# Kernel optimization log

Measured on AMD Instinct MI355X. Metric: run time of the kernel, lower is better.

The kernel has to match this reference:

```python
import math
import jax, jax.numpy as jnp
import numpy as np

ROUNDS = 4
BUCKET_LEN = 64
NEG_BIG = -1e9
NEG_SELF = -1e5
EPS = 1e-12


def look_back(x):
    # x: [B, n_buckets, bucket_len, ...]; prepend previous bucket (circular) along bucket_len axis
    return jnp.concatenate([jnp.roll(x, 1, axis=1), x], axis=2)


def gather_dim1(x, idx):
    # torch expand_gather: broadcast x and idx to common shape, gather along axis 1
    shape = np.broadcast_shapes(x.shape, idx.shape)
    return jnp.take_along_axis(jnp.broadcast_to(x, shape), jnp.broadcast_to(idx, shape), axis=1)


def setup_inputs() -> dict:
    key = jax.random.key(0)
    k1, k2, k3 = jax.random.split(key, 3)
    B, L, d_k = 16, 4096, 64
    n_buckets = L // BUCKET_LEN
    query = jax.random.normal(k1, (B, L, d_k), dtype=jnp.float32)
    value = jax.random.normal(k2, (B, L, d_k), dtype=jnp.float32)
    rand_matrix = jax.random.normal(k3, (B, d_k, ROUNDS, n_buckets // 2), dtype=jnp.float32)
    return {"query": query, "value": value, "rand_matrix": rand_matrix, "seed": 0}


def lsh_hashes(query, rand_matrix):
    # LocalitySensitiveHash.forward
    B, L, d_k = query.shape
    qn = query / jnp.maximum(jnp.linalg.norm(query, axis=-1, keepdims=True), EPS)
    rm = rand_matrix / jnp.linalg.norm(rand_matrix, axis=1, keepdims=True)
    mm = jnp.einsum('bld,bdrn->blrn', qn, rm)  # [B, L, rounds, n_buckets//2]
    h = jnp.argmax(jnp.concatenate([mm, -mm], axis=-1), axis=-1).astype(jnp.int32)  # [B, L, rounds]
    return h * L + jnp.arange(L, dtype=jnp.int32)[None, :, None]  # unique per position


def _lsh_attention(query, value, rand_matrix):
    B, L, d_k = query.shape
    R, bl = ROUNDS, BUCKET_LEN
    nb = L // bl

    h = lsh_hashes(query, rand_matrix)
    sorted_hashes = jnp.sort(h, axis=1)
    hash_indice = jnp.argsort(h, axis=1)               # [B, L, R]
    original_indice = jnp.argsort(hash_indice, axis=1)  # reverse_sort

    # reorder queries by hash, bucketize: [B, nb, bl, d_k, R]
    rq = gather_dim1(query[:, :, :, None], hash_indice[:, :, None, :]).reshape(B, nb, bl, d_k, R)
    lb_key = look_back(rq)
    lb_key = lb_key / jnp.maximum(jnp.linalg.norm(lb_key, axis=-2, keepdims=True), EPS)
    scores = jnp.einsum('bnidr,bnjdr->bnijr', rq, lb_key) / math.sqrt(d_k)  # [B, nb, bl, 2bl, R]

    # mask: different buckets, causal, self
    sh = sorted_hashes.reshape(B, nb, bl, R) // L  # bucket id
    scores = jnp.where(sh[..., None, :] != look_back(sh)[..., None, :, :], NEG_BIG, scores)
    qi = hash_indice.reshape(B, nb, bl, R).astype(jnp.int32)
    ki = look_back(qi)  # [B, nb, 2bl, R]
    scores = jnp.where(qi[..., None, :] < ki[..., None, :, :], NEG_BIG, scores)
    scores = jnp.where(qi[..., None, :] == ki[..., None, :, :], NEG_SELF, scores)

    # duplicate-key counting across rounds (get_dup_keys)
    ki_full = jnp.broadcast_to(ki[:, :, None, :, :], (B, nb, bl, 2 * bl, R)).reshape(B, L, 2 * bl, R)
    ki_full = gather_dim1(ki_full, original_indice[:, :, None, :])
    flat = ki_full.reshape(B, L, 2 * bl * R)
    s_idx = jnp.argsort(flat, axis=-1)
    s = jnp.take_along_axis(flat, s_idx, axis=-1)
    counts = jnp.ones_like(s)
    for i in range(1, R):
        eq = (s[..., i:] == s[..., :-i]).astype(s.dtype)
        counts = counts + jnp.pad(eq, ((0, 0), (0, 0), (i, 0))) + jnp.pad(eq, ((0, 0), (0, 0), (0, i)))
    inv = jnp.argsort(s_idx, axis=-1)
    count_key = jnp.take_along_axis(counts, inv, axis=-1).reshape(B, L, 2 * bl, R)
    count_key = gather_dim1(count_key, hash_indice[:, :, None, :])

    # duplicate-adjusted softmax
    scores = scores.reshape(B, L, 2 * bl, R)
    lse = jax.nn.logsumexp(scores, axis=2)  # [B, L, R]
    softmax_qk = jnp.exp(scores - jnp.log(count_key.astype(scores.dtype)) - lse[:, :, None, :])

    rv = gather_dim1(value[:, :, :, None], hash_indice[:, :, None, :]).reshape(B, nb, bl, d_k, R)
    sm = softmax_qk.reshape(B, nb, bl, 2 * bl, R)
    attn = jnp.einsum('bnijr,bnjdr->bnidr', sm, look_back(rv)).reshape(B, L, d_k, R)
    attn = gather_dim1(attn, original_indice[:, :, None, :])
    lse = jnp.take_along_axis(lse, original_indice, axis=1)
    round_weights = jax.nn.softmax(lse, axis=1)  # dim=1 (length) exactly as in the source
    return jnp.einsum('bldr,blr->bld', attn, round_weights)


def reference(query, value, rand_matrix, seed):
    # seed is unused by the original forward body; dropout skipped (eval mode)
    return _lsh_attention(query, value, rand_matrix)
```

## Files before the change

### kernel.cpp

```cpp
#include <hip/hip_runtime.h>
#include <math.h>

#define B_  16
#define L_  4096
#define D_  64
#define R_  4
#define NB_ 64
#define BL_ 64
#define FIXCAP 8192

typedef _Float16 f16x8 __attribute__((ext_vector_type(8)));
typedef _Float16 f16x2 __attribute__((ext_vector_type(2)));
typedef float    f32x4 __attribute__((ext_vector_type(4)));


__global__ __launch_bounds__(64) void k_rmnorm(const float* __restrict__ rm,
                                               double* __restrict__ rmn,
                                               _Float16* __restrict__ rhi_g,
                                               _Float16* __restrict__ rlo_g,
                                               int* __restrict__ fix_cnt) {
    if (blockIdx.x == 0 && threadIdx.x == 0) *fix_cnt = 0;
    int blk = blockIdx.x;
    int b = blk >> 7, r = (blk >> 5) & 3, n = blk & 31;
    int d = threadIdx.x;
    double v = (double)rm[(((size_t)b * 64 + d) * 4 + r) * 32 + n];
    double sq = v * v;
    #pragma unroll
    for (int off = 32; off > 0; off >>= 1) sq += __shfl_down(sq, off);
    double tot = __shfl(sq, 0);
    double nv = v / sqrt(tot);
    rmn[(((size_t)b * 4 + r) * 32 + n) * 64 + d] = nv;
    float f = (float)nv;
    _Float16 hi = (_Float16)f;
    size_t gi = ((size_t)b * 128 + r * 32 + n) * 64 + d;
    rhi_g[gi] = hi;
    rlo_g[gi] = (_Float16)(f - (float)hi);
}

__global__ __launch_bounds__(256, 4) void k_hash(const float* __restrict__ q,
                                                 const float* __restrict__ value,
                                                 const _Float16* __restrict__ rhi_g,
                                                 const _Float16* __restrict__ rlo_g,
                                                 int* __restrict__ h_ws,
                                                 int* __restrict__ fix_cnt,
                                                 int* __restrict__ fix_list,
                                                 _Float16* __restrict__ qhf,
                                                 _Float16* __restrict__ khf,
                                                 _Float16* __restrict__ vhf) {
    __shared__ __align__(16) char smem[36864];
    _Float16* Rhi = (_Float16*)smem;
    _Float16* Rlo = (_Float16*)(smem + 18432);
    float*    Sc  = (float*)smem;

    int blk = blockIdx.x;
    int b = blk >> 6, chunk = blk & 63;
    int tid = threadIdx.x;
    int w = tid >> 6, lane = tid & 63, quad = lane >> 4, l15 = lane & 15;

    {
        int row = chunk * 64 + (tid >> 2), sub = tid & 3;
        const float4* vp = (const float4*)(value + ((size_t)(b * L_ + row)) * 64 + sub * 16);
        f16x8 h0, h1;
        #pragma unroll
        for (int c = 0; c < 2; c++) {
            float4 t0 = vp[2 * c], t1 = vp[2 * c + 1];
            f16x8& hd = c ? h1 : h0;
            hd[0]=(_Float16)t0.x; hd[1]=(_Float16)t0.y; hd[2]=(_Float16)t0.z; hd[3]=(_Float16)t0.w;
            hd[4]=(_Float16)t1.x; hd[5]=(_Float16)t1.y; hd[6]=(_Float16)t1.z; hd[7]=(_Float16)t1.w;
        }
        _Float16* dst = vhf + ((size_t)(b * L_ + row)) * 64 + sub * 16;
        *(f16x8*)dst = h0;
        *(f16x8*)(dst + 8) = h1;
    }

    {
        int row = tid >> 1, dh = (tid & 1) * 32;
        const _Float16* sh = rhi_g + ((size_t)b * 128 + row) * 64 + dh;
        const _Float16* sl = rlo_g + ((size_t)b * 128 + row) * 64 + dh;
        #pragma unroll
        for (int g = 0; g < 4; g++) {
            *(f16x8*)&Rhi[row * 72 + dh + g * 8] = *(const f16x8*)(sh + g * 8);
            *(f16x8*)&Rlo[row * 72 + dh + g * 8] = *(const f16x8*)(sl + g * 8);
        }
    }

    int qrow = chunk * 64 + w * 16 + l15;
    const float* qp = q + ((size_t)(b * L_ + qrow)) * 64;
    float qv[16];
    #pragma unroll
    for (int kt = 0; kt < 2; kt++) {
        float4 t0 = *(const float4*)(qp + kt * 32 + quad * 8);
        float4 t1 = *(const float4*)(qp + kt * 32 + quad * 8 + 4);
        qv[8*kt+0]=t0.x; qv[8*kt+1]=t0.y; qv[8*kt+2]=t0.z; qv[8*kt+3]=t0.w;
        qv[8*kt+4]=t1.x; qv[8*kt+5]=t1.y; qv[8*kt+6]=t1.z; qv[8*kt+7]=t1.w;
    }
    f16x8 Ahi[2], Alo[2];
    #pragma unroll
    for (int kt = 0; kt < 2; kt++) {
        #pragma unroll
        for (int j = 0; j < 8; j++) {
            _Float16 hi = (_Float16)qv[8*kt+j];
            Ahi[kt][j] = hi;
            Alo[kt][j] = (_Float16)(qv[8*kt+j] - (float)hi);
        }
    }
    {
        float ss = 0.f;
        #pragma unroll
        for (int j = 0; j < 16; j++) ss += qv[j] * qv[j];
        ss += __shfl_xor(ss, 16);
        ss += __shfl_xor(ss, 32);
        float nr = sqrtf(ss); if (nr < 1e-12f) nr = 1e-12f;
        float kscale = 0.125f / nr;
        _Float16* qd = qhf + ((size_t)(b * L_ + qrow)) * 64;
        _Float16* kd = khf + ((size_t)(b * L_ + qrow)) * 64;
        #pragma unroll
        for (int kt = 0; kt < 2; kt++) {
            *(f16x8*)(qd + kt * 32 + quad * 8) = Ahi[kt];
            f16x8 hv;
            #pragma unroll
            for (int j = 0; j < 8; j++) hv[j] = (_Float16)(qv[8*kt+j] * kscale);
            *(f16x8*)(kd + kt * 32 + quad * 8) = hv;
        }
    }
    __syncthreads();

    f32x4 acc[8];
    #pragma unroll
    for (int jt = 0; jt < 8; jt++) acc[jt] = (f32x4){0.f, 0.f, 0.f, 0.f};
    #pragma unroll
    for (int jt = 0; jt < 8; jt++) {
        #pragma unroll
        for (int kt = 0; kt < 2; kt++) {
            f16x8 bh = *(const f16x8*)&Rhi[(jt * 16 + l15) * 72 + kt * 32 + quad * 8];
            f16x8 bl = *(const f16x8*)&Rlo[(jt * 16 + l15) * 72 + kt * 32 + quad * 8];
            acc[jt] = __builtin_amdgcn_mfma_f32_16x16x32_f16(Ahi[kt], bh, acc[jt], 0, 0, 0);
            acc[jt] = __builtin_amdgcn_mfma_f32_16x16x32_f16(Ahi[kt], bl, acc[jt], 0, 0, 0);
            acc[jt] = __builtin_amdgcn_mfma_f32_16x16x32_f16(Alo[kt], bh, acc[jt], 0, 0, 0);
        }
    }
    __syncthreads();

    #pragma unroll
    for (int jt = 0; jt < 8; jt++) {
        #pragma unroll
        for (int reg = 0; reg < 4; reg++)
            Sc[(w * 16 + quad * 4 + reg) * 133 + jt * 16 + l15] = acc[jt][reg];
    }
    __syncthreads();

    {
        int row = tid & 63, r = tid >> 6;
        const float* sp = &Sc[row * 133 + r * 32];
        float bp = -1e30f, bn = -1e30f; int ip = 0, in2 = 0;
        float v1 = -1e30f, v2 = -1e30f;
        #pragma unroll
        for (int n = 0; n < 32; n++) {
            float v = sp[n], nv = -v;
            if (v > bp)  { bp = v;  ip = n; }
            if (nv > bn) { bn = nv; in2 = n; }
            if (v > v1)       { v2 = v1; v1 = v; }
            else if (v > v2)  { v2 = v; }
            if (nv > v1)      { v2 = v1; v1 = nv; }
            else if (nv > v2) { v2 = nv; }
        }
        int i1 = (bp >= bn) ? ip : (32 + in2);
        int l = chunk * 64 + row;
        h_ws[((size_t)(b * 4 + r)) * L_ + l] = i1;
        if (v1 - v2 < 4e-5f) {
            int slot = atomicAdd(fix_cnt, 1);
            if (slot < FIXCAP) fix_list[slot] = (b << 14) | (r << 12) | l;
        }
    }
}

__global__ __launch_bounds__(64) void k_fix(const float* __restrict__ q,
                                            const double* __restrict__ rmn,
                                            const int* __restrict__ fix_cnt,
                                            const int* __restrict__ fix_list,
                                            int* __restrict__ h_ws) {
    int cnt = *fix_cnt; if (cnt > FIXCAP) cnt = FIXCAP;
    int lane = threadIdx.x;
    for (int i = blockIdx.x; i < cnt; i += gridDim.x) {
        int e = fix_list[i];
        int b = e >> 14, r = (e >> 12) & 3, l = e & 4095;
        int n = lane & 31;
        const double* rp = rmn + ((size_t)(b * 4 + r)) * 2048 + n * 64;
        const float* qr = q + ((size_t)(b * L_ + l)) * 64;
        double a0 = 0.0, a1 = 0.0, a2 = 0.0, a3 = 0.0;
        #pragma unroll
        for (int d = 0; d < 64; d += 4) {
            a0 += (double)qr[d]   * rp[d];
            a1 += (double)qr[d+1] * rp[d+1];
            a2 += (double)qr[d+2] * rp[d+2];
            a3 += (double)qr[d+3] * rp[d+3];
        }
        double acc = ((a0 + a1) + (a2 + a3));
        double v = (lane < 32) ? acc : -acc;
        int idx = lane;
        #pragma unroll
        for (int off = 1; off < 64; off <<= 1) {
            double ov = __shfl_xor(v, off);
            int   oidx = __shfl_xor(idx, off);
            if (ov > v || (ov == v && oidx < idx)) { v = ov; idx = oidx; }
        }
        if (lane == 0) h_ws[((size_t)(b * 4 + r)) * L_ + l] = idx;
    }
}

__global__ __launch_bounds__(64) void k_sort(const int* __restrict__ h_ws,
                                             int* __restrict__ hi_ws,
                                             int* __restrict__ oi_ws) {
    __shared__ int hs[64 * 65];
    __shared__ int cnt[64 * 65];
    int br = blockIdx.x;
    const int* hp = h_ws + (size_t)br * L_;
    int t = threadIdx.x;
    for (int w = 0; w < 64; w++) hs[w * 65 + t] = hp[w * 64 + t];
    for (int u = 0; u < 64; u++) cnt[t * 65 + u] = 0;
    __syncthreads();
    for (int k = 0; k < 64; k++) cnt[t * 65 + hs[t * 65 + k]]++;
    __syncthreads();
    int cs = 0;
    for (int c = 0; c < 64; c++) cs += cnt[c * 65 + t];
    int v = cs;
    #pragma unroll
    for (int off = 1; off < 64; off <<= 1) {
        int u = __shfl_up(v, off);
        if (t >= off) v += u;
    }
    int running = v - cs;
    for (int c = 0; c < 64; c++) {
        int tmp = cnt[c * 65 + t];
        cnt[c * 65 + t] = running;
        running += tmp;
    }
    __syncthreads();
    int* hi = hi_ws + (size_t)br * L_;
    int* oi = oi_ws + (size_t)br * L_;
    for (int k = 0; k < 64; k++) {
        int idx = t * 64 + k;
        int b2 = hs[t * 65 + k];
        int pos = cnt[t * 65 + b2]++;
        hi[pos] = idx;
        oi[idx] = pos;
    }
}

__global__ __launch_bounds__(256) void k_meta(const int* __restrict__ h_ws,
                                              const int* __restrict__ hi_ws,
                                              const int* __restrict__ oi_ws,
                                              int4* __restrict__ meta_ws) {
    int gid = blockIdx.x * 256 + threadIdx.x;
    int br = gid >> 12, spos = gid & 4095;
    int b = br >> 2;
    int p = hi_ws[(size_t)br * L_ + spos];
    int hh = h_ws[(size_t)br * L_ + p];
    int pack = 0, packm1 = 0;
    #pragma unroll
    for (int r2 = 0; r2 < 4; r2++) {
        int bk = oi_ws[((size_t)(b * 4 + r2)) * L_ + p] >> 6;
        pack   |= bk << (8 * r2);
        packm1 |= ((bk + 63) & 63) << (8 * r2);
    }
    meta_ws[(size_t)br * L_ + spos] = make_int4(hh, p, pack, packm1);
}

__global__ __launch_bounds__(256, 4) void k_attn(const _Float16* __restrict__ qhf,
                                                 const _Float16* __restrict__ khf,
                                                 const _Float16* __restrict__ vhf,
                                                 const int4* __restrict__ meta_ws,
                                                 float* __restrict__ lse_ws,
                                                 _Float16* __restrict__ attn_ws) {
    __shared__ _Float16 Ksh[128 * 72];
    __shared__ _Float16 Vt[64 * 136];
    __shared__ int4 kmeta[128];

    int xcd = blockIdx.x & 7, slot = blockIdx.x >> 3;
    int b = xcd * 2 + (slot >> 8);
    int rem = slot & 255, n = rem >> 2, r = rem & 3;
    int tid = threadIdx.x;
    int w = tid >> 6, lane = tid & 63, quad = lane >> 4, l15 = lane & 15;
    int hibase = (b * 4 + r) * L_;

    if (tid < 128) {
        int j = tid;
        int nprev = (n + 63) & 63;
        int spos = (j < 64) ? (nprev * 64 + j) : (n * 64 + (j - 64));
        kmeta[j] = meta_ws[hibase + spos];
    }
    __syncthreads();

    {
        int j = tid >> 1, dh = (tid & 1) * 32;
        const _Float16* src = khf + ((size_t)(b * L_ + kmeta[j].y)) * 64 + dh;
        #pragma unroll
        for (int g = 0; g < 4; g++)
            *(f16x8*)&Ksh[j * 72 + dh + g * 8] = *(const f16x8*)(src + g * 8);
    }
    {
        int m = tid >> 2, sub = tid & 3;
        const _Float16* v0 = vhf + ((size_t)(b * L_ + kmeta[2 * m].y)) * 64 + sub * 16;
        const _Float16* v1 = vhf + ((size_t)(b * L_ + kmeta[2 * m + 1].y)) * 64 + sub * 16;
        f16x8 a00 = *(const f16x8*)v0, a01 = *(const f16x8*)(v0 + 8);
        f16x8 a10 = *(const f16x8*)v1, a11 = *(const f16x8*)(v1 + 8);
        #pragma unroll
        for (int d = 0; d < 8; d++) {
            f16x2 hv = { a00[d], a10[d] };
            *(f16x2*)&Vt[(sub * 16 + d) * 136 + 2 * m] = hv;
            f16x2 hw = { a01[d], a11[d] };
            *(f16x2*)&Vt[(sub * 16 + 8 + d) * 136 + 2 * m] = hw;
        }
    }

    int4 qmw = kmeta[64 + w * 16 + l15];
    const _Float16* qp = qhf + ((size_t)(b * L_ + qmw.y)) * 64;
    f16x8 afr[2];
    afr[0] = *(const f16x8*)(qp + quad * 8);
    afr[1] = *(const f16x8*)(qp + 32 + quad * 8);
    __syncthreads();

    f32x4 acc[8];
    #pragma unroll
    for (int jt = 0; jt < 8; jt++) acc[jt] = (f32x4){0.f, 0.f, 0.f, 0.f};
    #pragma unroll
    for (int jt = 0; jt < 8; jt++) {
        #pragma unroll
        for (int kt = 0; kt < 2; kt++) {
            f16x8 bfr = *(const f16x8*)&Ksh[(jt * 16 + l15) * 72 + kt * 32 + quad * 8];
            acc[jt] = __builtin_amdgcn_mfma_f32_16x16x32_f16(afr[kt], bfr, acc[jt], 0, 0, 0);
        }
    }

    int4 qm4[4], km4[8];
    #pragma unroll
    for (int reg = 0; reg < 4; reg++) qm4[reg] = kmeta[64 + w * 16 + quad * 4 + reg];
    #pragma unroll
    for (int jt = 0; jt < 8; jt++) km4[jt] = kmeta[jt * 16 + l15];
    __syncthreads();

    _Float16* Ph = Ksh;
    float lse_r[4];
    #pragma unroll
    for (int reg = 0; reg < 4; reg++) {
        float s[8];
        #pragma unroll
        for (int jt = 0; jt < 8; jt++) {
            float v = acc[jt][reg];
            if (km4[jt].x != qm4[reg].x) v = -1e9f;
            if (qm4[reg].y < km4[jt].y)  v = -1e9f;
            if (qm4[reg].y == km4[jt].y) v = -1e5f;
            s[jt] = v;
        }
        float m = s[0];
        #pragma unroll
        for (int jt = 1; jt < 8; jt++) m = fmaxf(m, s[jt]);
        #pragma unroll
        for (int off = 1; off < 16; off <<= 1) m = fmaxf(m, __shfl_xor(m, off));
        float te[8], sum = 0.f;
        #pragma unroll
        for (int jt = 0; jt < 8; jt++) { te[jt] = __expf(s[jt] - m); sum += te[jt]; }
        #pragma unroll
        for (int off = 1; off < 16; off <<= 1) sum += __shfl_xor(sum, off);
        float inv = __builtin_amdgcn_rcpf(sum);
        lse_r[reg] = m + __logf(sum);
        int i = w * 16 + quad * 4 + reg;
        #pragma unroll
        for (int jt = 0; jt < 8; jt++) {
            int z1 = km4[jt].z ^ qm4[reg].z;
            int z2 = km4[jt].z ^ qm4[reg].w;
            int nz = __popc((z1 + 0x7f7f7f7f) & 0x80808080)
                   + __popc((z2 + 0x7f7f7f7f) & 0x80808080);
            float p = te[jt] * inv * __builtin_amdgcn_rcpf((float)(8 - nz));
            Ph[i * 136 + jt * 16 + l15] = (_Float16)p;
        }
    }
    if (l15 == 0) {
        #pragma unroll
        for (int reg = 0; reg < 4; reg++)
            lse_ws[hibase + qm4[reg].y] = lse_r[reg];
    }
    __syncthreads();

    f32x4 oacc[4];
    #pragma unroll
    for (int nt = 0; nt < 4; nt++) oacc[nt] = (f32x4){0.f, 0.f, 0.f, 0.f};
    #pragma unroll
    for (int kt = 0; kt < 4; kt++) {
        f16x8 pa = *(const f16x8*)&Ph[(w * 16 + l15) * 136 + kt * 32 + quad * 8];
        #pragma unroll
        for (int nt = 0; nt < 4; nt++) {
            f16x8 vb = *(const f16x8*)&Vt[(nt * 16 + l15) * 136 + kt * 32 + quad * 8];
            oacc[nt] = __builtin_amdgcn_mfma_f32_16x16x32_f16(pa, vb, oacc[nt], 0, 0, 0);
        }
    }
    #pragma unroll
    for (int reg = 0; reg < 4; reg++) {
        size_t base = (((size_t)(b * 4 + r)) * L_ + qm4[reg].y) * 64;
        #pragma unroll
        for (int nt = 0; nt < 4; nt++)
            attn_ws[base + nt * 16 + l15] = (_Float16)oacc[nt][reg];
    }
}

__global__ __launch_bounds__(256) void k_rw(const float* __restrict__ lse_ws,
                                            float* __restrict__ rwmax,
                                            float* __restrict__ rwsum) {
    __shared__ float  red[256];
    __shared__ double redd[256];
    int br = blockIdx.x;
    const float* lp = lse_ws + (size_t)br * L_;
    int t = threadIdx.x;
    float m = -1e30f;
    for (int k = t; k < L_; k += 256) m = fmaxf(m, lp[k]);
    red[t] = m; __syncthreads();
    for (int s2 = 128; s2 > 0; s2 >>= 1) {
        if (t < s2) red[t] = fmaxf(red[t], red[t + s2]);
        __syncthreads();
    }
    float mm = red[0];
    double s = 0.0;
    for (int k = t; k < L_; k += 256) s += (double)expf(lp[k] - mm);
    redd[t] = s; __syncthreads();
    for (int s2 = 128; s2 > 0; s2 >>= 1) {
        if (t < s2) redd[t] += redd[t + s2];
        __syncthreads();
    }
    if (t == 0) { rwmax[br] = mm; rwsum[br] = (float)redd[0]; }
}

__global__ __launch_bounds__(256) void k_out(const _Float16* __restrict__ attn_ws,
                                             const float* __restrict__ lse_ws,
                                             const float* __restrict__ rwmax,
                                             const float* __restrict__ rwsum,
                                             float* __restrict__ out) {
    int gid = blockIdx.x * 256 + threadIdx.x;
    int g = gid & 7;
    size_t row = (size_t)(gid >> 3);
    int b = (int)(row >> 12), l = (int)(row & 4095);
    float o[8];
    #pragma unroll
    for (int k = 0; k < 8; k++) o[k] = 0.f;
    #pragma unroll
    for (int r = 0; r < 4; r++) {
        int br = b * 4 + r;
        float wgt = __expf(lse_ws[(size_t)br * L_ + l] - rwmax[br])
                  * __builtin_amdgcn_rcpf(rwsum[br]);
        f16x8 av = *(const f16x8*)&attn_ws[(((size_t)br * L_ + l) << 6) + g * 8];
        #pragma unroll
        for (int k = 0; k < 8; k++) o[k] += (float)av[k] * wgt;
    }
    float4* op = (float4*)(out + row * 64 + g * 8);
    op[0] = make_float4(o[0], o[1], o[2], o[3]);
    op[1] = make_float4(o[4], o[5], o[6], o[7]);
}

extern "C" void kernel_launch(void* const* d_in, const int* in_sizes, int n_in,
                              void* d_out, int out_size, void* d_ws, size_t ws_size,
                              hipStream_t stream) {
    const float* query = (const float*)d_in[0];
    const float* value = (const float*)d_in[1];
    const float* rm    = (const float*)d_in[2];
    char* ws = (char*)d_ws;
    double*    rmn    = (double*)ws;
    int*       h_ws   = (int*)(ws + ((size_t)1 << 20));
    int*       hi_ws  = (int*)(ws + ((size_t)2 << 20));
    int*       oi_ws  = (int*)(ws + ((size_t)3 << 20));
    float*     lse_ws = (float*)(ws + ((size_t)4 << 20));
    float*     rwmax  = (float*)(ws + ((size_t)5 << 20));
    float*     rwsum  = (float*)(ws + ((size_t)5 << 20) + 256);
    int*       fix_cnt= (int*)(ws + ((size_t)5 << 20) + 512);
    int*       fix_list=(int*)(ws + ((size_t)5 << 20) + 1024);
    _Float16*  attn_ws= (_Float16*)(ws + ((size_t)6 << 20));
    _Float16*  rhi_g  = (_Float16*)(ws + ((size_t)40 << 20));
    _Float16*  rlo_g  = (_Float16*)(ws + ((size_t)40 << 20) + ((size_t)1 << 19));
    int4*      meta_ws= (int4*)(ws + ((size_t)41 << 20));
    _Float16*  qhf    = (_Float16*)(ws + ((size_t)45 << 20));
    _Float16*  khf    = (_Float16*)(ws + ((size_t)53 << 20));
    _Float16*  vhf    = (_Float16*)(ws + ((size_t)61 << 20));
    float*     out    = (float*)d_out;

    hipLaunchKernelGGL(k_rmnorm, dim3(2048), dim3(64),  0, stream, rm, rmn, rhi_g, rlo_g, fix_cnt);
    hipLaunchKernelGGL(k_hash,   dim3(1024), dim3(256), 0, stream, query, value, rhi_g, rlo_g,
                       h_ws, fix_cnt, fix_list, qhf, khf, vhf);
    hipLaunchKernelGGL(k_fix,    dim3(64),   dim3(64),  0, stream, query, rmn,
                       fix_cnt, fix_list, h_ws);
    hipLaunchKernelGGL(k_sort,   dim3(64),   dim3(64),  0, stream, h_ws, hi_ws, oi_ws);
    hipLaunchKernelGGL(k_meta,   dim3(1024), dim3(256), 0, stream, h_ws, hi_ws, oi_ws, meta_ws);
    hipLaunchKernelGGL(k_attn,   dim3(4096), dim3(256), 0, stream,
                       qhf, khf, vhf, meta_ws, lse_ws, attn_ws);
    hipLaunchKernelGGL(k_rw,     dim3(64),   dim3(256), 0, stream, lse_ws, rwmax, rwsum);
    hipLaunchKernelGGL(k_out,    dim3(2048), dim3(256), 0, stream,
                       attn_ws, lse_ws, rwmax, rwsum, out);
}
```

Measured before the change: 170.4 us.

## Parallelize counting sort, scatter meta, simplify argmax, use exp2 softmax with deferred normalization

The counting sort moves from 64 to 256 threads per block, using 16-bit shared-memory counters and a two-level prefix sum, and it no longer writes the hash-index array. k_meta now scatters metadata to sorted positions using the inverse permutation. The hash argmax becomes a branchless abs/sign-bit selection with fmed3 for tracking the runner-up. The attention softmax is moved to base 2 by pre-scaling keys by log2(e) and using exp2, and the 1/sum normalization is deferred to the output store. k_attn also reads key metadata straight from global memory instead of waiting on a shared-memory barrier. Together these aim to cut serial sort time, instruction counts and one barrier, at the cost of a scattered write pattern in k_meta and small numeric differences.

```diff
diff --git a/kernel.cpp b/kernel.cpp
--- a/kernel.cpp
+++ b/kernel.cpp
@@ -111,7 +111,7 @@
         ss += __shfl_xor(ss, 16);
         ss += __shfl_xor(ss, 32);
         float nr = sqrtf(ss); if (nr < 1e-12f) nr = 1e-12f;
-        float kscale = 0.125f / nr;
+        float kscale = 0.18033688f / nr;
         _Float16* qd = qhf + ((size_t)(b * L_ + qrow)) * 64;
         _Float16* kd = khf + ((size_t)(b * L_ + qrow)) * 64;
         #pragma unroll
@@ -152,19 +152,16 @@
     {
         int row = tid & 63, r = tid >> 6;
         const float* sp = &Sc[row * 133 + r * 32];
-        float bp = -1e30f, bn = -1e30f; int ip = 0, in2 = 0;
-        float v1 = -1e30f, v2 = -1e30f;
+        float v1 = -1e30f, v2 = -1e30f; int i1 = 0;
         #pragma unroll
         for (int n = 0; n < 32; n++) {
-            float v = sp[n], nv = -v;
-            if (v > bp)  { bp = v;  ip = n; }
-            if (nv > bn) { bn = nv; in2 = n; }
-            if (v > v1)       { v2 = v1; v1 = v; }
-            else if (v > v2)  { v2 = v; }
-            if (nv > v1)      { v2 = v1; v1 = nv; }
-            else if (nv > v2) { v2 = nv; }
-        }
-        int i1 = (bp >= bn) ? ip : (32 + in2);
+            float v = sp[n];
+            float a = fabsf(v);
+            int cand = n | ((__float_as_uint(v) >> 26) & 32);
+            if (a > v1) i1 = cand;
+            v2 = __builtin_amdgcn_fmed3f(a, v1, v2);
+            v1 = fmaxf(a, v1);
+        }
         int l = chunk * 64 + row;
         h_ws[((size_t)(b * 4 + r)) * L_ + l] = i1;
         if (v1 - v2 < 4e-5f) {
@@ -208,62 +205,107 @@
     }
 }
 
-__global__ __launch_bounds__(64) void k_sort(const int* __restrict__ h_ws,
-                                             int* __restrict__ hi_ws,
-                                             int* __restrict__ oi_ws) {
-    __shared__ int hs[64 * 65];
-    __shared__ int cnt[64 * 65];
+__global__ __launch_bounds__(256) void k_sort(const int* __restrict__ h_ws,
+                                              int* __restrict__ oi_ws) {
+    __shared__ __align__(16) unsigned short cnt[64 * 257];
+    __shared__ __align__(16) unsigned short oi_s[256 * 17];
+    __shared__ int part[256];
+
     int br = blockIdx.x;
+    int t = threadIdx.x;
     const int* hp = h_ws + (size_t)br * L_;
-    int t = threadIdx.x;
-    for (int w = 0; w < 64; w++) hs[w * 65 + t] = hp[w * 64 + t];
-    for (int u = 0; u < 64; u++) cnt[t * 65 + u] = 0;
-    __syncthreads();
-    for (int k = 0; k < 64; k++) cnt[t * 65 + hs[t * 65 + k]]++;
-    __syncthreads();
-    int cs = 0;
-    for (int c = 0; c < 64; c++) cs += cnt[c * 65 + t];
-    int v = cs;
-    #pragma unroll
-    for (int off = 1; off < 64; off <<= 1) {
-        int u = __shfl_up(v, off);
-        if (t >= off) v += u;
-    }
-    int running = v - cs;
-    for (int c = 0; c < 64; c++) {
-        int tmp = cnt[c * 65 + t];
-        cnt[c * 65 + t] = running;
-        running += tmp;
-    }
-    __syncthreads();
-    int* hi = hi_ws + (size_t)br * L_;
-    int* oi = oi_ws + (size_t)br * L_;
-    for (int k = 0; k < 64; k++) {
-        int idx = t * 64 + k;
-        int b2 = hs[t * 65 + k];
-        int pos = cnt[t * 65 + b2]++;
-        hi[pos] = idx;
-        oi[idx] = pos;
+
+    unsigned int* cz = (unsigned int*)cnt;
+    #pragma unroll
+    for (int i = 0; i < 33; i++) {
+        int idx = i * 256 + t;
+        if (idx < 8224) cz[idx] = 0;
+    }
+
+    int key[16];
+    const int4* hp4 = (const int4*)(hp + t * 16);
+    #pragma unroll
+    for (int g = 0; g < 4; g++) {
+        int4 v = hp4[g];
+        key[g*4+0] = v.x; key[g*4+1] = v.y; key[g*4+2] = v.z; key[g*4+3] = v.w;
+    }
+    __syncthreads();
+
+    #pragma unroll
+    for (int k = 0; k < 16; k++) {
+        unsigned short* c = &cnt[key[k] * 257 + t];
+        *c = (unsigned short)(*c + 1);
+    }
+    __syncthreads();
+
+    int u = t & 63, s = t >> 6;
+    {
+        int run = 0;
+        int base_idx = u * 257 + s * 64;
+        #pragma unroll 16
+        for (int i = 0; i < 64; i++) {
+            int c = cnt[base_idx + i];
+            cnt[base_idx + i] = (unsigned short)run;
+            run += c;
+        }
+        part[s * 64 + u] = run;
+    }
+    __syncthreads();
+
+    if (t < 64) {
+        int p0 = part[t], p1 = part[64 + t], p2 = part[128 + t], p3 = part[192 + t];
+        int tot = p0 + p1 + p2 + p3;
+        int v = tot;
+        #pragma unroll
+        for (int off = 1; off < 64; off <<= 1) {
+            int o = __shfl_up(v, off);
+            if (t >= off) v += o;
+        }
+        int base = v - tot;
+        part[t]       = base;
+        part[64 + t]  = base + p0;
+        part[128 + t] = base + p0 + p1;
+        part[192 + t] = base + p0 + p1 + p2;
+    }
+    __syncthreads();
+
+    int sbase = s * 64;
+    #pragma unroll
+    for (int k = 0; k < 16; k++) {
+        int uk = key[k];
+        unsigned short* c = &cnt[uk * 257 + t];
+        int pos = part[sbase + uk] + *c;
+        *c = (unsigned short)(*c + 1);
+        int idx = t * 16 + k;
+        oi_s[(idx >> 4) * 17 + (idx & 15)] = (unsigned short)pos;
+    }
+    __syncthreads();
+
+    int* op = oi_ws + (size_t)br * L_;
+    #pragma unroll
+    for (int k = 0; k < 16; k++) {
+        int e = k * 256 + t;
+        op[e] = (int)oi_s[(e >> 4) * 17 + (e & 15)];
     }
 }
 
 __global__ __launch_bounds__(256) void k_meta(const int* __restrict__ h_ws,
-                                              const int* __restrict__ hi_ws,
                                               const int* __restrict__ oi_ws,
                                               int4* __restrict__ meta_ws) {
     int gid = blockIdx.x * 256 + threadIdx.x;
-    int br = gid >> 12, spos = gid & 4095;
-    int b = br >> 2;
-    int p = hi_ws[(size_t)br * L_ + spos];
+    int br = gid >> 12, p = gid & 4095;
+    int b = br >> 2, rme = br & 3;
     int hh = h_ws[(size_t)br * L_ + p];
-    int pack = 0, packm1 = 0;
+    int pack = 0, packm1 = 0, mypos = 0;
     #pragma unroll
     for (int r2 = 0; r2 < 4; r2++) {
-        int bk = oi_ws[((size_t)(b * 4 + r2)) * L_ + p] >> 6;
+        int o = oi_ws[((size_t)(b * 4 + r2)) * L_ + p];
+        if (r2 == rme) mypos = o;
+        int bk = o >> 6;
         pack   |= bk << (8 * r2);
         packm1 |= ((bk + 63) & 63) << (8 * r2);
     }
-    meta_ws[(size_t)br * L_ + spos] = make_int4(hh, p, pack, packm1);
+    meta_ws[(size_t)br * L_ + mypos] = make_int4(hh, p, pack, packm1);
 }
 
 __global__ __launch_bounds__(256, 4) void k_attn(const _Float16* __restrict__ qhf,
@@ -282,26 +324,31 @@
     int tid = threadIdx.x;
     int w = tid >> 6, lane = tid & 63, quad = lane >> 4, l15 = lane & 15;
     int hibase = (b * 4 + r) * L_;
+    const int4* mp = meta_ws + hibase;
+    int nprev = (n + 63) & 63;
 
     if (tid < 128) {
         int j = tid;
-        int nprev = (n + 63) & 63;
         int spos = (j < 64) ? (nprev * 64 + j) : (n * 64 + (j - 64));
-        kmeta[j] = meta_ws[hibase + spos];
-    }
-    __syncthreads();
-
+        kmeta[j] = mp[spos];
+    }
     {
         int j = tid >> 1, dh = (tid & 1) * 32;
-        const _Float16* src = khf + ((size_t)(b * L_ + kmeta[j].y)) * 64 + dh;
+        int spos = (j < 64) ? (nprev * 64 + j) : (n * 64 + (j - 64));
+        int ky = mp[spos].y;
+        const _Float16* src = khf + ((size_t)(b * L_ + ky)) * 64 + dh;
         #pragma unroll
         for (int g = 0; g < 4; g++)
             *(f16x8*)&Ksh[j * 72 + dh + g * 8] = *(const f16x8*)(src + g * 8);
     }
     {
         int m = tid >> 2, sub = tid & 3;
-        const _Float16* v0 = vhf + ((size_t)(b * L_ + kmeta[2 * m].y)) * 64 + sub * 16;
-        const _Float16* v1 = vhf + ((size_t)(b * L_ + kmeta[2 * m + 1].y)) * 64 + sub * 16;
+        int j0 = 2 * m, j1 = 2 * m + 1;
+        int sp0 = (j0 < 64) ? (nprev * 64 + j0) : (n * 64 + (j0 - 64));
+        int sp1 = (j1 < 64) ? (nprev * 64 + j1) : (n * 64 + (j1 - 64));
+        int y0 = mp[sp0].y, y1 = mp[sp1].y;
+        const _Float16* v0 = vhf + ((size_t)(b * L_ + y0)) * 64 + sub * 16;
+        const _Float16* v1 = vhf + ((size_t)(b * L_ + y1)) * 64 + sub * 16;
         f16x8 a00 = *(const f16x8*)v0, a01 = *(const f16x8*)(v0 + 8);
         f16x8 a10 = *(const f16x8*)v1, a11 = *(const f16x8*)(v1 + 8);
         #pragma unroll
@@ -313,8 +360,8 @@
         }
     }
 
-    int4 qmw = kmeta[64 + w * 16 + l15];
-    const _Float16* qp = qhf + ((size_t)(b * L_ + qmw.y)) * 64;
+    int qy = mp[n * 64 + w * 16 + l15].y;
+    const _Float16* qp = qhf + ((size_t)(b * L_ + qy)) * 64;
     f16x8 afr[2];
     afr[0] = *(const f16x8*)(qp + quad * 8);
     afr[1] = *(const f16x8*)(qp + 32 + quad * 8);
@@ -340,16 +387,16 @@
     __syncthreads();
 
     _Float16* Ph = Ksh;
-    float lse_r[4];
+    float lse_r[4], inv_r[4];
     #pragma unroll
     for (int reg = 0; reg < 4; reg++) {
         float s[8];
         #pragma unroll
         for (int jt = 0; jt < 8; jt++) {
             float v = acc[jt][reg];
-            if (km4[jt].x != qm4[reg].x) v = -1e9f;
-            if (qm4[reg].y < km4[jt].y)  v = -1e9f;
-            if (qm4[reg].y == km4[jt].y) v = -1e5f;
+            if (km4[jt].x != qm4[reg].x) v = -1.4426951e9f;
+            if (qm4[reg].y < km4[jt].y)  v = -1.4426951e9f;
+            if (qm4[reg].y == km4[jt].y) v = -144269.50f;
             s[jt] = v;
         }
         float m = s[0];
@@ -359,11 +406,11 @@
         for (int off = 1; off < 16; off <<= 1) m = fmaxf(m, __shfl_xor(m, off));
         float te[8], sum = 0.f;
         #pragma unroll
-        for (int jt = 0; jt < 8; jt++) { te[jt] = __expf(s[jt] - m); sum += te[jt]; }
+        for (int jt = 0; jt < 8; jt++) { te[jt] = __builtin_amdgcn_exp2f(s[jt] - m); sum += te[jt]; }
         #pragma unroll
         for (int off = 1; off < 16; off <<= 1) sum += __shfl_xor(sum, off);
-        float inv = __builtin_amdgcn_rcpf(sum);
-        lse_r[reg] = m + __logf(sum);
+        inv_r[reg] = __builtin_amdgcn_rcpf(sum);
+        lse_r[reg] = m * 0.6931472f + __logf(sum);
         int i = w * 16 + quad * 4 + reg;
         #pragma unroll
         for (int jt = 0; jt < 8; jt++) {
@@ -371,7 +418,7 @@
             int z2 = km4[jt].z ^ qm4[reg].w;
             int nz = __popc((z1 + 0x7f7f7f7f) & 0x80808080)
                    + __popc((z2 + 0x7f7f7f7f) & 0x80808080);
-            float p = te[jt] * inv * __builtin_amdgcn_rcpf((float)(8 - nz));
+            float p = te[jt] * __builtin_amdgcn_rcpf((float)(8 - nz));
             Ph[i * 136 + jt * 16 + l15] = (_Float16)p;
         }
     }
@@ -399,7 +446,7 @@
         size_t base = (((size_t)(b * 4 + r)) * L_ + qm4[reg].y) * 64;
         #pragma unroll
         for (int nt = 0; nt < 4; nt++)
-            attn_ws[base + nt * 16 + l15] = (_Float16)oacc[nt][reg];
+            attn_ws[base + nt * 16 + l15] = (_Float16)(oacc[nt][reg] * inv_r[reg]);
     }
 }
 
@@ -464,7 +511,6 @@
     char* ws = (char*)d_ws;
     double*    rmn    = (double*)ws;
     int*       h_ws   = (int*)(ws + ((size_t)1 << 20));
-    int*       hi_ws  = (int*)(ws + ((size_t)2 << 20));
     int*       oi_ws  = (int*)(ws + ((size_t)3 << 20));
     float*     lse_ws = (float*)(ws + ((size_t)4 << 20));
     float*     rwmax  = (float*)(ws + ((size_t)5 << 20));
@@ -485,8 +531,8 @@
                        h_ws, fix_cnt, fix_list, qhf, khf, vhf);
     hipLaunchKernelGGL(k_fix,    dim3(64),   dim3(64),  0, stream, query, rmn,
                        fix_cnt, fix_list, h_ws);
-    hipLaunchKernelGGL(k_sort,   dim3(64),   dim3(64),  0, stream, h_ws, hi_ws, oi_ws);
-    hipLaunchKernelGGL(k_meta,   dim3(1024), dim3(256), 0, stream, h_ws, hi_ws, oi_ws, meta_ws);
+    hipLaunchKernelGGL(k_sort,   dim3(64),   dim3(256), 0, stream, h_ws, oi_ws);
+    hipLaunchKernelGGL(k_meta,   dim3(1024), dim3(256), 0, stream, h_ws, oi_ws, meta_ws);
     hipLaunchKernelGGL(k_attn,   dim3(4096), dim3(256), 0, stream,
                        qhf, khf, vhf, meta_ws, lse_ws, attn_ws);
     hipLaunchKernelGGL(k_rw,     dim3(64),   dim3(256), 0, stream, lse_ws, rwmax, rwsum);
```

Measured after the change: 164.6 us. -3.4%, faster.
